# Optimization experiments

Hardware: AMD Instinct MI355X
Metric: run time of the kernel (lower is better)

Reference implementation:

```python
import jax, jax.numpy as jnp
import numpy as np

N = 512       # n_nodes (also number of per-node attention heads)
F_IN = 256    # n_feature
H = 64        # h_feature
C = 64        # n_class (must equal H for V * out broadcast)
K = 12        # top-K threshold for learned adjacency
ALPHA = 0.2   # LeakyReLU negative slope


def setup_inputs() -> dict:
    key = jax.random.key(0)
    ks = jax.random.split(key, 6)
    X = jax.random.normal(ks[0], (N, F_IN), jnp.float32)
    # stacked params of the n_nodes first-layer attention heads
    W_stack = jax.random.normal(ks[1], (N, F_IN, H), jnp.float32) * 0.05
    a_stack = jax.random.normal(ks[2], (N, 2 * H, 1), jnp.float32) * 0.05
    # output attention layer: in_Channel = h_feature * n_nodes
    W_out = jax.random.normal(ks[3], (H * N, C), jnp.float32) * 0.02
    a_out = jax.random.normal(ks[4], (2 * C, 1), jnp.float32) * 0.05
    V = jax.random.normal(ks[5], (N, H), jnp.float32) * 0.1
    return {"X": X, "W_stack": W_stack, "a_stack": a_stack,
            "W_out": W_out, "a_out": a_out, "V": V}


def gat_layer(Hx, adj, W, a):
    # Faithful to Graph_Attention_Covlayer.forward, but the O(N^2 * 2F)
    # concat tensor is algebraically collapsed: concat(Wh[i], Wh[j]) @ a
    # == (Wh @ a1)[i] + (Wh @ a2)[j], a broadcast sum.
    Wh = Hx @ W                      # (N, F)
    f = W.shape[1]
    e1 = Wh @ a[:f, 0]               # (N,)
    e2 = Wh @ a[f:, 0]               # (N,)
    S = jax.nn.leaky_relu(e1[:, None] + e2[None, :], ALPHA)  # (N, N)
    A = jax.nn.softmax(S, axis=1)    # softmax BEFORE masking, as in source
    A = jnp.where(adj > 0, A, jnp.zeros_like(A))
    out = A @ Wh                     # (N, F)
    return jax.nn.elu(out)           # concat=True -> elu


def adj_learn(V):
    A = V @ V.T                      # (N, N)
    kth = jax.lax.top_k(A.reshape(-1), K)[0][-1]
    # source: Adj = 1 where A > kth-value, else 0 (strict >)
    return jnp.where(A > kth, jnp.ones_like(A), jnp.zeros_like(A))


def reference(X, W_stack, a_stack, W_out, a_out, V):
    adj = adj_learn(V)
    # all n_nodes heads share input X and adj -> vmap over stacked params
    heads = jax.vmap(lambda W, a: gat_layer(X, adj, W, a))(W_stack, a_stack)  # (N_heads, N, H)
    # torch.cat(..., dim=1): row i = [head0_feats | head1_feats | ...]
    mid = jnp.transpose(heads, (1, 0, 2)).reshape(N, N * H)
    # dropout: eval mode -> identity
    out = gat_layer(mid, adj, W_out, a_out)  # (N, C)
    out = jax.nn.elu(V * out)
    return adj, out
```

## Files before the change

kernel.cpp:

```cpp
#include <hip/hip_runtime.h>


#define XT_OFF    0
#define CAND_OFF  131072
#define KTH_OFF   134144
#define INT_OFF   134208
#define MIDC_OFF  134400
#define PART_OFF  527616
#define I_CNT   0
#define I_ENT   8
#define I_M     24
#define I_R     25
#define I_ROWS  32
#define I_ER    48
#define I_EJ    64
#define I_ECJ   80

__device__ __forceinline__ float leaky_(float x) { return fmaxf(x, 0.2f * x); }
__device__ __forceinline__ float elu_(float x)   { return x > 0.f ? x : __expf(x) - 1.f; }

__global__ void k1_prep(const float* __restrict__ V, const float* __restrict__ X,
                        float* __restrict__ wsf, float* __restrict__ out) {
  int b = blockIdx.x, t = threadIdx.x;
  if (b < 512) {
    __shared__ float vi[64];
    if (t < 64) vi[t] = V[b * 64 + t];
    __syncthreads();
    #pragma unroll
    for (int jj = 0; jj < 2; ++jj) {
      int j = t + jj * 256;
      const float4* vj = reinterpret_cast<const float4*>(V + j * 64);
      float acc = 0.f;
      #pragma unroll
      for (int q = 0; q < 16; ++q) {
        float4 v4 = vj[q];
        acc += v4.x * vi[q*4] + v4.y * vi[q*4+1] + v4.z * vi[q*4+2] + v4.w * vi[q*4+3];
      }
      out[b * 512 + j] = acc;
    }
  } else if (b < 640) {
    int base = (b - 512) * 1024;
    #pragma unroll
    for (int q = 0; q < 4; ++q) {
      int o = base + q * 256 + t;
      int f = o >> 9, j = o & 511;
      wsf[XT_OFF + o] = X[j * 256 + f];
    }
  } else {
    int base = 262144 + (b - 640) * 512 + t;
    out[base] = 0.f;
    out[base + 256] = 0.f;
    if (b == 640 && t == 0) {
      int* ip = (int*)(wsf + INT_OFF);
      ip[I_CNT] = 0;
    }
  }
}

__global__ void k2_topk_block(const float* __restrict__ A, float* __restrict__ wsf) {
  __shared__ float svw[4]; __shared__ int siw[4];
  int b = blockIdx.x, t = threadIdx.x;
  int l = t & 63, w = t >> 6;
  float4 v4 = *reinterpret_cast<const float4*>(A + b * 1024 + t * 4);
  float v0 = v4.x, v1 = v4.y, v2 = v4.z, v3 = v4.w;
  for (int round = 0; round < 12; ++round) {
    float m = v0; int mi = 0;
    if (v1 > m) { m = v1; mi = 1; }
    if (v2 > m) { m = v2; mi = 2; }
    if (v3 > m) { m = v3; mi = 3; }
    int idx = (t << 2) | mi;
    #pragma unroll
    for (int d = 1; d < 64; d <<= 1) {
      float ov = __shfl_xor(m, d);
      int   oi = __shfl_xor(idx, d);
      if (ov > m || (ov == m && oi < idx)) { m = ov; idx = oi; }
    }
    if (l == 0) { svw[w] = m; siw[w] = idx; }
    __syncthreads();
    float bm = svw[0]; int bi = siw[0];
    #pragma unroll
    for (int ww = 1; ww < 4; ++ww) {
      if (svw[ww] > bm || (svw[ww] == bm && siw[ww] < bi)) { bm = svw[ww]; bi = siw[ww]; }
    }
    if (t == 0) wsf[CAND_OFF + b * 12 + round] = bm;
    if ((bi >> 2) == t) {
      int q = bi & 3;
      if (q == 0) v0 = -INFINITY; else if (q == 1) v1 = -INFINITY;
      else if (q == 2) v2 = -INFINITY; else v3 = -INFINITY;
    }
    __syncthreads();
  }
}

__global__ void k3_topk_final(float* __restrict__ wsf) {
  __shared__ float svw[4]; __shared__ int siw[4];
  int t = threadIdx.x, l = t & 63, w = t >> 6;
  float v[12];
  #pragma unroll
  for (int q = 0; q < 12; ++q) v[q] = wsf[CAND_OFF + t * 12 + q];
  unsigned rm = 0;
  float kth = 0.f;
  for (int round = 0; round < 12; ++round) {
    float m = -INFINITY; int mi = 0;
    #pragma unroll
    for (int q = 0; q < 12; ++q) {
      bool ok = ((rm >> q) & 1u) == 0u;
      if (ok && v[q] > m) { m = v[q]; mi = q; }
    }
    int idx = (t << 4) | mi;
    #pragma unroll
    for (int d = 1; d < 64; d <<= 1) {
      float ov = __shfl_xor(m, d);
      int   oi = __shfl_xor(idx, d);
      if (ov > m || (ov == m && oi < idx)) { m = ov; idx = oi; }
    }
    if (l == 0) { svw[w] = m; siw[w] = idx; }
    __syncthreads();
    float bm = svw[0]; int bi = siw[0];
    #pragma unroll
    for (int ww = 1; ww < 4; ++ww) {
      if (svw[ww] > bm || (svw[ww] == bm && siw[ww] < bi)) { bm = svw[ww]; bi = siw[ww]; }
    }
    if ((bi >> 4) == t) rm |= 1u << (bi & 15);
    kth = bm;
    __syncthreads();
  }
  if (t == 0) wsf[KTH_OFF] = kth;
}

__global__ void k4_adj(float* __restrict__ outAdj, float* __restrict__ wsf) {
  int b = blockIdx.x, t = threadIdx.x;
  float kth = wsf[KTH_OFF];
  int* ip = (int*)(wsf + INT_OFF);
  int base = b * 1024 + t * 4;
  float4 a = *reinterpret_cast<const float4*>(outAdj + base);
  float va[4] = { a.x, a.y, a.z, a.w };
  float ov[4];
  #pragma unroll
  for (int q = 0; q < 4; ++q) {
    bool one = va[q] > kth;
    ov[q] = one ? 1.f : 0.f;
    if (one) {
      int pos = atomicAdd(&ip[I_CNT], 1);
      if (pos < 12) ip[I_ENT + pos] = base + q;
    }
  }
  float4 o; o.x = ov[0]; o.y = ov[1]; o.z = ov[2]; o.w = ov[3];
  *reinterpret_cast<float4*>(outAdj + base) = o;
}

__global__ void k5_finalize(float* __restrict__ wsf) {
  if (threadIdx.x != 0) return;
  int* ip = (int*)(wsf + INT_OFF);
  int cnt = ip[I_CNT];
  if (cnt > 12) cnt = 12;
  if (cnt < 0)  cnt = 0;
  int e[12];
  for (int m = 0; m < cnt; ++m) e[m] = ip[I_ENT + m];
  for (int a = 1; a < cnt; ++a) {
    int key = e[a]; int b = a - 1;
    while (b >= 0 && e[b] > key) { e[b + 1] = e[b]; --b; }
    e[b + 1] = key;
  }
  int R = 0; int rows[12], er_[12], ej_[12];
  for (int m = 0; m < cnt; ++m) {
    int i2 = e[m] >> 9, j2 = e[m] & 511;
    if (R == 0 || rows[R - 1] != i2) rows[R++] = i2;
    er_[m] = R - 1; ej_[m] = j2;
  }
  ip[I_M] = cnt; ip[I_R] = R;
  for (int r = 0; r < 12; ++r) ip[I_ROWS + r] = (r < R) ? rows[r] : 0;
  for (int m = 0; m < 12; ++m) {
    ip[I_ER + m] = (m < cnt) ? er_[m] : 0;
    ip[I_EJ + m] = (m < cnt) ? ej_[m] : 0;
    int cj = -1;
    if (m < cnt) { for (int r = 0; r < R; ++r) if (rows[r] == ej_[m]) cj = r; }
    ip[I_ECJ + m] = cj;
  }
}

__global__ __launch_bounds__(256, 4) void k6_heads(
    const float* __restrict__ X, const float* __restrict__ Wst,
    const float* __restrict__ ast, float* __restrict__ wsf) {
  __shared__ int   shdr[96];
  __shared__ float al[128];
  __shared__ float w1[256], w2[256];
  __shared__ __align__(16) float XeT[256 * 12];
  __shared__ float whp[4][768];
  __shared__ float wh_ent[768];
  __shared__ float e2s[512];
  __shared__ float e1r[12], mr[12], sr[12], avals[12];
  __shared__ float red4[48], redw[4];

  int h = blockIdx.x, t = threadIdx.x;
  int l = t & 63, w = t >> 6;
  const int* ip = (const int*)(wsf + INT_OFF);
  if (t < 96)  shdr[t] = ip[t];
  if (t < 128) al[t] = ast[h * 128 + t];
  __syncthreads();
  int M = shdr[I_M], R = shdr[I_R];
  const float* Wb = Wst + h * 16384;

  {
    int fg = l >> 4;
    int kc = (l & 15) << 2;
    #pragma unroll 4
    for (int it = 0; it < 16; ++it) {
      int f = w * 64 + it * 4 + fg;
      float4 wq = *reinterpret_cast<const float4*>(Wb + f * 64 + kc);
      float p1 = wq.x * al[kc] + wq.y * al[kc+1] + wq.z * al[kc+2] + wq.w * al[kc+3];
      float p2 = wq.x * al[64+kc] + wq.y * al[64+kc+1] + wq.z * al[64+kc+2] + wq.w * al[64+kc+3];
      #pragma unroll
      for (int d = 1; d < 16; d <<= 1) { p1 += __shfl_xor(p1, d); p2 += __shfl_xor(p2, d); }
      if ((l & 15) == 0) { w1[f] = p1; w2[f] = p2; }
    }
  }
  #pragma unroll
  for (int m = 0; m < 12; ++m) {
    float v = 0.f;
    if (m < M) v = X[shdr[I_EJ + m] * 256 + t];
    XeT[t * 12 + m] = v;
  }
  __syncthreads();

  {
    float wh[12];
    #pragma unroll
    for (int m = 0; m < 12; ++m) wh[m] = 0.f;
    const float* Wb2 = Wb + w * 4096;
    #pragma unroll 2
    for (int i = 0; i < 64; ++i) {
      float wv = Wb2[i * 64 + l];
      const float4* xr = reinterpret_cast<const float4*>(&XeT[(w * 64 + i) * 12]);
      float4 xa = xr[0], xb = xr[1], xc = xr[2];
      wh[0] += xa.x * wv; wh[1] += xa.y * wv; wh[2]  += xa.z * wv; wh[3]  += xa.w * wv;
      wh[4] += xb.x * wv; wh[5] += xb.y * wv; wh[6]  += xb.z * wv; wh[7]  += xb.w * wv;
      wh[8] += xc.x * wv; wh[9] += xc.y * wv; wh[10] += xc.z * wv; wh[11] += xc.w * wv;
    }
    #pragma unroll
    for (int m = 0; m < 12; ++m) whp[w][m * 64 + l] = wh[m];
  }

  for (int r = w; r < R; r += 4) {
    int row = shdr[I_ROWS + r];
    float p = 0.f;
    #pragma unroll
    for (int s = 0; s < 4; ++s) {
      int f = s * 64 + l;
      p += X[row * 256 + f] * w1[f];
    }
    #pragma unroll
    for (int d = 1; d < 64; d <<= 1) p += __shfl_xor(p, d);
    if (l == 0) e1r[r] = p;
  }

  {
    const float2* XT2 = reinterpret_cast<const float2*>(wsf + XT_OFF);
    float a0 = 0.f, a1 = 0.f;
    #pragma unroll 4
    for (int f = 0; f < 256; ++f) {
      float2 xv = XT2[f * 256 + t];
      float wf = w2[f];
      a0 += xv.x * wf; a1 += xv.y * wf;
    }
    e2s[2 * t] = a0; e2s[2 * t + 1] = a1;
  }
  __syncthreads();

  for (int o = t, c = 0; c < 3; ++c, o += 256)
    wh_ent[o] = whp[0][o] + whp[1][o] + whp[2][o] + whp[3][o];
  {
    float p = fmaxf(e2s[w * 128 + l], e2s[w * 128 + 64 + l]);
    #pragma unroll
    for (int d = 1; d < 64; d <<= 1) p = fmaxf(p, __shfl_xor(p, d));
    if (l == 0) redw[w] = p;
  }
  __syncthreads();

  float maxe2 = fmaxf(fmaxf(redw[0], redw[1]), fmaxf(redw[2], redw[3]));
  for (int r = 0; r < R; ++r) {
    float e1_ = e1r[r];
    float m_ = leaky_(e1_ + maxe2);
    float pe = __expf(leaky_(e1_ + e2s[t]) - m_) + __expf(leaky_(e1_ + e2s[t + 256]) - m_);
    #pragma unroll
    for (int d = 1; d < 64; d <<= 1) pe += __shfl_xor(pe, d);
    if (l == 0) red4[r * 4 + w] = pe;
    if (t == r) mr[r] = m_;
  }
  __syncthreads();
  if (t < R) sr[t] = red4[t * 4] + red4[t * 4 + 1] + red4[t * 4 + 2] + red4[t * 4 + 3];
  __syncthreads();
  if (t < M) {
    int r = shdr[I_ER + t];
    avals[t] = __expf(leaky_(e1r[r] + e2s[shdr[I_EJ + t]]) - mr[r]) / sr[r];
  }
  __syncthreads();

  for (int r = w; r < R; r += 4) {
    float a = 0.f;
    #pragma unroll
    for (int m = 0; m < 12; ++m) {
      if (m < M && shdr[I_ER + m] == r) a += avals[m] * wh_ent[m * 64 + l];
    }
    wsf[MIDC_OFF + r * 32768 + h * 64 + l] = elu_(a);
  }
}

__global__ void k7_wh2(const float* __restrict__ Wout, float* __restrict__ wsf) {
  __shared__ __align__(16) float midT[256 * 12];
  __shared__ float whp[4][768];
  int b = blockIdx.x, t = threadIdx.x;
  int l = t & 63, w = t >> 6;
  const int* ip = (const int*)(wsf + INT_OFF);
  int R = ip[I_R];
  #pragma unroll
  for (int m = 0; m < 12; ++m) {
    float v = 0.f;
    if (m < R) v = wsf[MIDC_OFF + m * 32768 + b * 256 + t];
    midT[t * 12 + m] = v;
  }
  __syncthreads();
  float acc[12];
  #pragma unroll
  for (int m = 0; m < 12; ++m) acc[m] = 0.f;
  #pragma unroll 2
  for (int ci = 0; ci < 64; ++ci) {
    int cc = w * 64 + ci;
    float wv = Wout[(b * 256 + cc) * 64 + l];
    const float4* xr = reinterpret_cast<const float4*>(&midT[cc * 12]);
    float4 xa = xr[0], xb = xr[1], xc = xr[2];
    acc[0] += xa.x * wv; acc[1] += xa.y * wv; acc[2]  += xa.z * wv; acc[3]  += xa.w * wv;
    acc[4] += xb.x * wv; acc[5] += xb.y * wv; acc[6]  += xb.z * wv; acc[7]  += xb.w * wv;
    acc[8] += xc.x * wv; acc[9] += xc.y * wv; acc[10] += xc.z * wv; acc[11] += xc.w * wv;
  }
  #pragma unroll
  for (int m = 0; m < 12; ++m) whp[w][m * 64 + l] = acc[m];
  __syncthreads();
  for (int o = t, c = 0; c < 3; ++c, o += 256) {
    float s = whp[0][o] + whp[1][o] + whp[2][o] + whp[3][o];
    wsf[PART_OFF + o * 128 + b] = s;
  }
}

__global__ void k8_final(const float* __restrict__ aout, const float* __restrict__ V,
                         float* __restrict__ wsf, float* __restrict__ out) {
  __shared__ float Wh2[768];
  __shared__ float e1o[12], e2o[12], mr[12], sr[12], avals[12];
  int t = threadIdx.x;
  const int* ip = (const int*)(wsf + INT_OFF);
  int M = ip[I_M], R = ip[I_R];
  for (int o = t, c = 0; c < 3; ++c, o += 256) {
    float s = 0.f;
    const float4* p4 = reinterpret_cast<const float4*>(wsf + PART_OFF + o * 128);
    #pragma unroll 4
    for (int q = 0; q < 32; ++q) { float4 v = p4[q]; s += v.x + v.y + v.z + v.w; }
    Wh2[o] = s;
  }
  __syncthreads();
  if (t < R) {
    float s1 = 0.f, s2 = 0.f;
    for (int k = 0; k < 64; ++k) {
      float wv = Wh2[t * 64 + k];
      s1 += wv * aout[k];
      s2 += wv * aout[64 + k];
    }
    e1o[t] = s1; e2o[t] = s2;
  }
  __syncthreads();
  if (t < R) {
    float maxe = 0.f;
    for (int r = 0; r < R; ++r) maxe = fmaxf(maxe, e2o[r]);
    float m_ = leaky_(e1o[t] + maxe);
    float s = (float)(512 - R) * __expf(leaky_(e1o[t]) - m_);
    for (int r = 0; r < R; ++r) s += __expf(leaky_(e1o[t] + e2o[r]) - m_);
    mr[t] = m_; sr[t] = s;
  }
  __syncthreads();
  if (t < M) {
    int r = ip[I_ER + t];
    int cj = ip[I_ECJ + t];
    float e2v = (cj >= 0) ? e2o[cj] : 0.f;
    avals[t] = __expf(leaky_(e1o[r] + e2v) - mr[r]) / sr[r];
  }
  __syncthreads();
  int l = t & 63, w = t >> 6;
  for (int r = w; r < R; r += 4) {
    float a = 0.f;
    #pragma unroll
    for (int m = 0; m < 12; ++m) {
      if (m < M && ip[I_ER + m] == r) {
        int cj = ip[I_ECJ + m];
        float wv = (cj >= 0) ? Wh2[cj * 64 + l] : 0.f;
        a += avals[m] * wv;
      }
    }
    int row = ip[I_ROWS + r];
    float o2 = elu_(a);
    out[262144 + row * 64 + l] = elu_(V[row * 64 + l] * o2);
  }
}

extern "C" void kernel_launch(void* const* d_in, const int* in_sizes, int n_in,
                              void* d_out, int out_size, void* d_ws, size_t ws_size,
                              hipStream_t stream) {
  const float* X    = (const float*)d_in[0];
  const float* Wst  = (const float*)d_in[1];
  const float* ast  = (const float*)d_in[2];
  const float* Wout = (const float*)d_in[3];
  const float* aout = (const float*)d_in[4];
  const float* V    = (const float*)d_in[5];
  float* out = (float*)d_out;
  float* wsf = (float*)d_ws;

  k1_prep      <<<704, 256, 0, stream>>>(V, X, wsf, out);
  k2_topk_block<<<256, 256, 0, stream>>>(out, wsf);
  k3_topk_final<<<1,   256, 0, stream>>>(wsf);
  k4_adj       <<<256, 256, 0, stream>>>(out, wsf);
  k5_finalize  <<<1,    64, 0, stream>>>(wsf);
  k6_heads     <<<512, 256, 0, stream>>>(X, Wst, ast, wsf);
  k7_wh2       <<<128, 256, 0, stream>>>(Wout, wsf);
  k8_final     <<<1,   256, 0, stream>>>(aout, V, wsf, out);
}
```

Baseline: 134.4 us.

## Split per-head kernel and compute e2 scores with a tiled shared-memory GEMM

The monolithic per-head kernel becomes three stages. A weight pass reads W once to get both the attention projections and the entry-row Wh products. A tiled 64x64 GEMM then computes e2 = X·w2 for all heads together, split over four K-chunks. A stats kernel finishes the masked softmax. The top-k block pass now uses one wave with 16 values per lane and a bitmask, removing block-level syncs, and the X transpose prep is dropped. The aim is to stop every head streaming the whole transposed X. The cost is two extra launches and partial results written to and reread from workspace.

```diff
diff --git a/kernel.cpp b/kernel.cpp
--- a/kernel.cpp
+++ b/kernel.cpp
@@ -1,12 +1,15 @@
 #include <hip/hip_runtime.h>
 
 
-#define XT_OFF    0
-#define CAND_OFF  131072
-#define KTH_OFF   134144
-#define INT_OFF   134208
-#define MIDC_OFF  134400
-#define PART_OFF  527616
+#define INT_OFF   0
+#define CAND_OFF  128
+#define KTH_OFF   3200
+#define W2_OFF    3264
+#define E1_OFF    134336
+#define WH_OFF    142528
+#define E2P_OFF   535744
+#define MIDC_OFF  1584320
+#define PART_OFF  535744
 #define I_CNT   0
 #define I_ENT   8
 #define I_M     24
@@ -19,8 +22,8 @@
 __device__ __forceinline__ float leaky_(float x) { return fmaxf(x, 0.2f * x); }
 __device__ __forceinline__ float elu_(float x)   { return x > 0.f ? x : __expf(x) - 1.f; }
 
-__global__ void k1_prep(const float* __restrict__ V, const float* __restrict__ X,
-                        float* __restrict__ wsf, float* __restrict__ out) {
+__global__ void k1_prep(const float* __restrict__ V, float* __restrict__ wsf,
+                        float* __restrict__ out) {
   int b = blockIdx.x, t = threadIdx.x;
   if (b < 512) {
     __shared__ float vi[64];
@@ -38,19 +41,11 @@
       }
       out[b * 512 + j] = acc;
     }
-  } else if (b < 640) {
-    int base = (b - 512) * 1024;
-    #pragma unroll
-    for (int q = 0; q < 4; ++q) {
-      int o = base + q * 256 + t;
-      int f = o >> 9, j = o & 511;
-      wsf[XT_OFF + o] = X[j * 256 + f];
-    }
   } else {
-    int base = 262144 + (b - 640) * 512 + t;
+    int base = 262144 + (b - 512) * 512 + t;
     out[base] = 0.f;
     out[base + 256] = 0.f;
-    if (b == 640 && t == 0) {
+    if (b == 512 && t == 0) {
       int* ip = (int*)(wsf + INT_OFF);
       ip[I_CNT] = 0;
     }
@@ -58,37 +53,31 @@
 }
 
 __global__ void k2_topk_block(const float* __restrict__ A, float* __restrict__ wsf) {
-  __shared__ float svw[4]; __shared__ int siw[4];
-  int b = blockIdx.x, t = threadIdx.x;
-  int l = t & 63, w = t >> 6;
-  float4 v4 = *reinterpret_cast<const float4*>(A + b * 1024 + t * 4);
-  float v0 = v4.x, v1 = v4.y, v2 = v4.z, v3 = v4.w;
+  int b = blockIdx.x, l = threadIdx.x;
+  const float4* src = reinterpret_cast<const float4*>(A + b * 1024);
+  float v[16];
+  #pragma unroll
+  for (int u = 0; u < 4; ++u) {
+    float4 x = src[u * 64 + l];
+    v[u*4] = x.x; v[u*4+1] = x.y; v[u*4+2] = x.z; v[u*4+3] = x.w;
+  }
+  unsigned rm = 0;
   for (int round = 0; round < 12; ++round) {
-    float m = v0; int mi = 0;
-    if (v1 > m) { m = v1; mi = 1; }
-    if (v2 > m) { m = v2; mi = 2; }
-    if (v3 > m) { m = v3; mi = 3; }
-    int idx = (t << 2) | mi;
+    float m = -INFINITY; int mi = 0;
+    #pragma unroll
+    for (int q = 0; q < 16; ++q) {
+      bool ok = ((rm >> q) & 1u) == 0u;
+      if (ok && v[q] > m) { m = v[q]; mi = q; }
+    }
+    int idx = (l << 4) | mi;
     #pragma unroll
     for (int d = 1; d < 64; d <<= 1) {
       float ov = __shfl_xor(m, d);
       int   oi = __shfl_xor(idx, d);
       if (ov > m || (ov == m && oi < idx)) { m = ov; idx = oi; }
     }
-    if (l == 0) { svw[w] = m; siw[w] = idx; }
-    __syncthreads();
-    float bm = svw[0]; int bi = siw[0];
-    #pragma unroll
-    for (int ww = 1; ww < 4; ++ww) {
-      if (svw[ww] > bm || (svw[ww] == bm && siw[ww] < bi)) { bm = svw[ww]; bi = siw[ww]; }
-    }
-    if (t == 0) wsf[CAND_OFF + b * 12 + round] = bm;
-    if ((bi >> 2) == t) {
-      int q = bi & 3;
-      if (q == 0) v0 = -INFINITY; else if (q == 1) v1 = -INFINITY;
-      else if (q == 2) v2 = -INFINITY; else v3 = -INFINITY;
-    }
-    __syncthreads();
+    if (l == 0) wsf[CAND_OFF + b * 12 + round] = m;
+    if ((idx >> 4) == l) rm |= 1u << (idx & 15);
   }
 }
 
@@ -179,42 +168,19 @@
   }
 }
 
-__global__ __launch_bounds__(256, 4) void k6_heads(
+__global__ __launch_bounds__(256) void k6a_wpass(
     const float* __restrict__ X, const float* __restrict__ Wst,
     const float* __restrict__ ast, float* __restrict__ wsf) {
   __shared__ int   shdr[96];
-  __shared__ float al[128];
-  __shared__ float w1[256], w2[256];
+  __shared__ float w1l[256], w2l[256];
   __shared__ __align__(16) float XeT[256 * 12];
-  __shared__ float whp[4][768];
-  __shared__ float wh_ent[768];
-  __shared__ float e2s[512];
-  __shared__ float e1r[12], mr[12], sr[12], avals[12];
-  __shared__ float red4[48], redw[4];
-
+  __shared__ __align__(16) float whp[4][768];
   int h = blockIdx.x, t = threadIdx.x;
   int l = t & 63, w = t >> 6;
   const int* ip = (const int*)(wsf + INT_OFF);
-  if (t < 96)  shdr[t] = ip[t];
-  if (t < 128) al[t] = ast[h * 128 + t];
+  if (t < 96) shdr[t] = ip[t];
   __syncthreads();
   int M = shdr[I_M], R = shdr[I_R];
-  const float* Wb = Wst + h * 16384;
-
-  {
-    int fg = l >> 4;
-    int kc = (l & 15) << 2;
-    #pragma unroll 4
-    for (int it = 0; it < 16; ++it) {
-      int f = w * 64 + it * 4 + fg;
-      float4 wq = *reinterpret_cast<const float4*>(Wb + f * 64 + kc);
-      float p1 = wq.x * al[kc] + wq.y * al[kc+1] + wq.z * al[kc+2] + wq.w * al[kc+3];
-      float p2 = wq.x * al[64+kc] + wq.y * al[64+kc+1] + wq.z * al[64+kc+2] + wq.w * al[64+kc+3];
-      #pragma unroll
-      for (int d = 1; d < 16; d <<= 1) { p1 += __shfl_xor(p1, d); p2 += __shfl_xor(p2, d); }
-      if ((l & 15) == 0) { w1[f] = p1; w2[f] = p2; }
-    }
-  }
   #pragma unroll
   for (int m = 0; m < 12; ++m) {
     float v = 0.f;
@@ -223,52 +189,138 @@
   }
   __syncthreads();
 
-  {
-    float wh[12];
-    #pragma unroll
-    for (int m = 0; m < 12; ++m) wh[m] = 0.f;
-    const float* Wb2 = Wb + w * 4096;
-    #pragma unroll 2
-    for (int i = 0; i < 64; ++i) {
-      float wv = Wb2[i * 64 + l];
-      const float4* xr = reinterpret_cast<const float4*>(&XeT[(w * 64 + i) * 12]);
-      float4 xa = xr[0], xb = xr[1], xc = xr[2];
-      wh[0] += xa.x * wv; wh[1] += xa.y * wv; wh[2]  += xa.z * wv; wh[3]  += xa.w * wv;
-      wh[4] += xb.x * wv; wh[5] += xb.y * wv; wh[6]  += xb.z * wv; wh[7]  += xb.w * wv;
-      wh[8] += xc.x * wv; wh[9] += xc.y * wv; wh[10] += xc.z * wv; wh[11] += xc.w * wv;
-    }
-    #pragma unroll
-    for (int m = 0; m < 12; ++m) whp[w][m * 64 + l] = wh[m];
-  }
-
+  const float* Wb = Wst + h * 16384;
+  int fg = l >> 4, kc = (l & 15) << 2;
+  float4 a1q = *reinterpret_cast<const float4*>(ast + h * 128 + kc);
+  float4 a2q = *reinterpret_cast<const float4*>(ast + h * 128 + 64 + kc);
+  float wh[12][4];
+  #pragma unroll
+  for (int m = 0; m < 12; ++m) { wh[m][0] = wh[m][1] = wh[m][2] = wh[m][3] = 0.f; }
+
+  #pragma unroll 4
+  for (int it = 0; it < 16; ++it) {
+    int f = w * 64 + it * 4 + fg;
+    float4 wq = *reinterpret_cast<const float4*>(Wb + f * 64 + kc);
+    float p1 = wq.x*a1q.x + wq.y*a1q.y + wq.z*a1q.z + wq.w*a1q.w;
+    float p2 = wq.x*a2q.x + wq.y*a2q.y + wq.z*a2q.z + wq.w*a2q.w;
+    #pragma unroll
+    for (int d = 1; d < 16; d <<= 1) { p1 += __shfl_xor(p1, d); p2 += __shfl_xor(p2, d); }
+    if ((l & 15) == 0) { w1l[f] = p1; w2l[f] = p2; }
+    const float4* xr = reinterpret_cast<const float4*>(&XeT[f * 12]);
+    float4 xa = xr[0], xb = xr[1], xc = xr[2];
+    float xv[12] = { xa.x, xa.y, xa.z, xa.w, xb.x, xb.y, xb.z, xb.w,
+                     xc.x, xc.y, xc.z, xc.w };
+    #pragma unroll
+    for (int m = 0; m < 12; ++m) {
+      wh[m][0] += xv[m] * wq.x;
+      wh[m][1] += xv[m] * wq.y;
+      wh[m][2] += xv[m] * wq.z;
+      wh[m][3] += xv[m] * wq.w;
+    }
+  }
+  #pragma unroll
+  for (int m = 0; m < 12; ++m) {
+    #pragma unroll
+    for (int q = 0; q < 4; ++q) {
+      float x = wh[m][q];
+      x += __shfl_xor(x, 16);
+      x += __shfl_xor(x, 32);
+      wh[m][q] = x;
+    }
+  }
+  if (l < 16) {
+    #pragma unroll
+    for (int m = 0; m < 12; ++m) {
+      float4 vv = make_float4(wh[m][0], wh[m][1], wh[m][2], wh[m][3]);
+      *reinterpret_cast<float4*>(&whp[w][m * 64 + kc]) = vv;
+    }
+  }
+  __syncthreads();
+  #pragma unroll
+  for (int c = 0; c < 3; ++c) {
+    int o = c * 256 + t;
+    wsf[WH_OFF + h * 768 + o] = whp[0][o] + whp[1][o] + whp[2][o] + whp[3][o];
+  }
+  wsf[W2_OFF + h * 256 + t] = w2l[t];
   for (int r = w; r < R; r += 4) {
     int row = shdr[I_ROWS + r];
     float p = 0.f;
     #pragma unroll
     for (int s = 0; s < 4; ++s) {
       int f = s * 64 + l;
-      p += X[row * 256 + f] * w1[f];
+      p += X[row * 256 + f] * w1l[f];
     }
     #pragma unroll
     for (int d = 1; d < 64; d <<= 1) p += __shfl_xor(p, d);
-    if (l == 0) e1r[r] = p;
-  }
-
+    if (l == 0) wsf[E1_OFF + h * 16 + r] = p;
+  }
+}
+
+__global__ __launch_bounds__(256) void ke2_gemm(const float* __restrict__ X,
+                                                float* __restrict__ wsf) {
+  __shared__ __align__(16) float As[64][68];
+  __shared__ __align__(16) float Bs[64][68];
+  int b = blockIdx.x, t = threadIdx.x;
+  int q = b >> 6, bh = (b >> 3) & 7, bj = b & 7;
+  int r = t >> 2, c0 = (t & 3) * 16;
+  const float* wsrc = wsf + W2_OFF + (bh * 64 + r) * 256 + q * 64 + c0;
+  const float* xsrc = X + (bj * 64 + r) * 256 + q * 64 + c0;
+  #pragma unroll
+  for (int u = 0; u < 4; ++u) {
+    float4 a4 = *reinterpret_cast<const float4*>(wsrc + u * 4);
+    float4 b4 = *reinterpret_cast<const float4*>(xsrc + u * 4);
+    As[c0 + u*4 + 0][r] = a4.x; As[c0 + u*4 + 1][r] = a4.y;
+    As[c0 + u*4 + 2][r] = a4.z; As[c0 + u*4 + 3][r] = a4.w;
+    Bs[c0 + u*4 + 0][r] = b4.x; Bs[c0 + u*4 + 1][r] = b4.y;
+    Bs[c0 + u*4 + 2][r] = b4.z; Bs[c0 + u*4 + 3][r] = b4.w;
+  }
+  __syncthreads();
+  int th = t >> 4, tj = t & 15;
+  float acc[4][4] = {};
+  #pragma unroll 8
+  for (int f = 0; f < 64; ++f) {
+    float4 a4 = *reinterpret_cast<const float4*>(&As[f][th * 4]);
+    float4 b4 = *reinterpret_cast<const float4*>(&Bs[f][tj * 4]);
+    float av[4] = { a4.x, a4.y, a4.z, a4.w };
+    float bv[4] = { b4.x, b4.y, b4.z, b4.w };
+    #pragma unroll
+    for (int i = 0; i < 4; ++i)
+      #pragma unroll
+      for (int j = 0; j < 4; ++j)
+        acc[i][j] += av[i] * bv[j];
+  }
+  float* dst = wsf + E2P_OFF + q * 262144 + (bh * 64 + th * 4) * 512 + bj * 64 + tj * 4;
+  #pragma unroll
+  for (int i = 0; i < 4; ++i) {
+    float4 o4 = make_float4(acc[i][0], acc[i][1], acc[i][2], acc[i][3]);
+    *reinterpret_cast<float4*>(dst + i * 512) = o4;
+  }
+}
+
+__global__ void k6c_stats(float* __restrict__ wsf) {
+  __shared__ int   shdr[96];
+  __shared__ float e1r[12], whl[768], e2s[512];
+  __shared__ float redw[4], red4[48], mr[12], sr[12], avals[12];
+  int h = blockIdx.x, t = threadIdx.x, l = t & 63, w = t >> 6;
+  const int* ip = (const int*)(wsf + INT_OFF);
+  if (t < 96) shdr[t] = ip[t];
+  if (t >= 128 && t < 140) e1r[t - 128] = wsf[E1_OFF + h * 16 + (t - 128)];
+  #pragma unroll
+  for (int c = 0; c < 3; ++c) {
+    int o = c * 256 + t;
+    whl[o] = wsf[WH_OFF + h * 768 + o];
+  }
   {
-    const float2* XT2 = reinterpret_cast<const float2*>(wsf + XT_OFF);
-    float a0 = 0.f, a1 = 0.f;
-    #pragma unroll 4
-    for (int f = 0; f < 256; ++f) {
-      float2 xv = XT2[f * 256 + t];
-      float wf = w2[f];
-      a0 += xv.x * wf; a1 += xv.y * wf;
-    }
-    e2s[2 * t] = a0; e2s[2 * t + 1] = a1;
-  }
-  __syncthreads();
-
-  for (int o = t, c = 0; c < 3; ++c, o += 256)
-    wh_ent[o] = whp[0][o] + whp[1][o] + whp[2][o] + whp[3][o];
+    float s0 = 0.f, s1 = 0.f;
+    #pragma unroll
+    for (int qq = 0; qq < 4; ++qq) {
+      s0 += wsf[E2P_OFF + qq * 262144 + h * 512 + t];
+      s1 += wsf[E2P_OFF + qq * 262144 + h * 512 + 256 + t];
+    }
+    e2s[t] = s0; e2s[t + 256] = s1;
+  }
+  __syncthreads();
+  int M = shdr[I_M], R = shdr[I_R];
   {
     float p = fmaxf(e2s[w * 128 + l], e2s[w * 128 + 64 + l]);
     #pragma unroll
@@ -276,7 +328,6 @@
     if (l == 0) redw[w] = p;
   }
   __syncthreads();
-
   float maxe2 = fmaxf(fmaxf(redw[0], redw[1]), fmaxf(redw[2], redw[3]));
   for (int r = 0; r < R; ++r) {
     float e1_ = e1r[r];
@@ -295,12 +346,11 @@
     avals[t] = __expf(leaky_(e1r[r] + e2s[shdr[I_EJ + t]]) - mr[r]) / sr[r];
   }
   __syncthreads();
-
   for (int r = w; r < R; r += 4) {
     float a = 0.f;
     #pragma unroll
     for (int m = 0; m < 12; ++m) {
-      if (m < M && shdr[I_ER + m] == r) a += avals[m] * wh_ent[m * 64 + l];
+      if (m < M && shdr[I_ER + m] == r) a += avals[m] * whl[m * 64 + l];
     }
     wsf[MIDC_OFF + r * 32768 + h * 64 + l] = elu_(a);
   }
@@ -338,7 +388,7 @@
   __syncthreads();
   for (int o = t, c = 0; c < 3; ++c, o += 256) {
     float s = whp[0][o] + whp[1][o] + whp[2][o] + whp[3][o];
-    wsf[PART_OFF + o * 128 + b] = s;
+    wsf[PART_OFF + b * 768 + o] = s;
   }
 }
 
@@ -351,9 +401,8 @@
   int M = ip[I_M], R = ip[I_R];
   for (int o = t, c = 0; c < 3; ++c, o += 256) {
     float s = 0.f;
-    const float4* p4 = reinterpret_cast<const float4*>(wsf + PART_OFF + o * 128);
-    #pragma unroll 4
-    for (int q = 0; q < 32; ++q) { float4 v = p4[q]; s += v.x + v.y + v.z + v.w; }
+    #pragma unroll 8
+    for (int bb = 0; bb < 128; ++bb) s += wsf[PART_OFF + bb * 768 + o];
     Wh2[o] = s;
   }
   __syncthreads();
@@ -412,12 +461,14 @@
   float* out = (float*)d_out;
   float* wsf = (float*)d_ws;
 
-  k1_prep      <<<704, 256, 0, stream>>>(V, X, wsf, out);
-  k2_topk_block<<<256, 256, 0, stream>>>(out, wsf);
+  k1_prep      <<<576, 256, 0, stream>>>(V, wsf, out);
+  k2_topk_block<<<256,  64, 0, stream>>>(out, wsf);
   k3_topk_final<<<1,   256, 0, stream>>>(wsf);
   k4_adj       <<<256, 256, 0, stream>>>(out, wsf);
   k5_finalize  <<<1,    64, 0, stream>>>(wsf);
-  k6_heads     <<<512, 256, 0, stream>>>(X, Wst, ast, wsf);
+  k6a_wpass    <<<512, 256, 0, stream>>>(X, Wst, ast, wsf);
+  ke2_gemm     <<<256, 256, 0, stream>>>(X, wsf);
+  k6c_stats    <<<512, 256, 0, stream>>>(wsf);
   k7_wh2       <<<128, 256, 0, stream>>>(Wout, wsf);
   k8_final     <<<1,   256, 0, stream>>>(aout, V, wsf, out);
 }
```

Result: no change. 136.3 us (+1.4%).
